# Optimization experiments

Measured on AMD Instinct MI355X. Metric: run time of the kernel, lower is better.

Reference implementation:

```python
import jax, jax.numpy as jnp
import numpy as np

D_MODEL = 1024
N_HEADS = 16
HEAD_DIM = D_MODEL // N_HEADS
SCALE = HEAD_DIM ** -0.5
MIN_VAL = jnp.finfo(jnp.float32).min


def setup_inputs() -> dict:
    key = jax.random.key(0)
    ks = jax.random.split(key, 7)
    B, T = 1, 2048
    s = D_MODEL ** -0.5
    return {
        "x": jax.random.normal(ks[0], (B, T, D_MODEL), dtype=jnp.float32),
        "Wq": jax.random.normal(ks[1], (D_MODEL, D_MODEL), dtype=jnp.float32) * s,
        "Wk1": jax.random.normal(ks[2], (D_MODEL, D_MODEL), dtype=jnp.float32) * s,
        "Wk2": jax.random.normal(ks[3], (D_MODEL, D_MODEL), dtype=jnp.float32) * s,
        "Wv": jax.random.normal(ks[4], (D_MODEL, D_MODEL), dtype=jnp.float32) * s,
        "Wo": jax.random.normal(ks[5], (D_MODEL, D_MODEL), dtype=jnp.float32) * s,
        "lambda_logit": jnp.zeros((N_HEADS,), dtype=jnp.float32),  # logit(0.5)=0
    }


def _split_heads(y):
    B, T, _ = y.shape
    return y.reshape(B, T, N_HEADS, HEAD_DIM).transpose(0, 2, 1, 3)  # [B,H,T,hd]


def reference(x, Wq, Wk1, Wk2, Wv, Wo, lambda_logit):
    B, T, _ = x.shape
    q = _split_heads(x @ Wq.T)
    k1 = _split_heads(x @ Wk1.T)
    k2 = _split_heads(x @ Wk2.T)
    v = _split_heads(x @ Wv.T)

    s1 = jnp.einsum("bhqd,bhkd->bhqk", q, k1) * SCALE
    s2 = jnp.einsum("bhqd,bhkd->bhqk", q, k2) * SCALE

    causal = jnp.arange(T)[None, :] <= jnp.arange(T)[:, None]  # [T,T] keep mask
    s1 = jnp.where(causal[None, None], s1, MIN_VAL)
    s2 = jnp.where(causal[None, None], s2, MIN_VAL)

    attn_exp = jax.nn.softmax(s1, axis=-1)
    attn_noise = jax.nn.softmax(s2, axis=-1)
    lam = jax.nn.sigmoid(lambda_logit)[None, :, None, None]
    attn = attn_exp - lam * attn_noise
    denom = jnp.maximum(jnp.sum(jnp.abs(attn), axis=-1, keepdims=True), 1e-6)
    attn = attn / denom

    out = jnp.einsum("bhqk,bhkd->bhqd", attn, v)
    out = out.transpose(0, 2, 1, 3).reshape(B, T, D_MODEL)
    return out @ Wo.T
```

## Files before the change

### kernel.cpp

```cpp
#include <hip/hip_runtime.h>

#define T_SEQ 2048
#define DM 1024
#define NH 16
#define HD 64
#define SC2 0.1803368801111731f
#define LS 80

typedef unsigned short u16;
typedef unsigned int u32;
typedef __attribute__((ext_vector_type(8))) short bf16x8;
typedef __attribute__((ext_vector_type(4))) float f32x4;

static __device__ __forceinline__ f32x4 mfma16(bf16x8 a, bf16x8 b, f32x4 c) {
    return __builtin_amdgcn_mfma_f32_16x16x32_bf16(a, b, c, 0, 0, 0);
}
static __device__ __forceinline__ float bf2f(u16 u) {
    union { u32 i; float f; } v; v.i = ((u32)u) << 16; return v.f;
}
static __device__ __forceinline__ u16 f2bf(float f) {
    union { float f; u32 i; } v; v.f = f;
    u32 x = v.i;
    x += 0x7FFFu + ((x >> 16) & 1u);
    return (u16)(x >> 16);
}
static __device__ __forceinline__ u16 f2bf_t(float f) {
    union { float f; u32 i; } v; v.f = f;
    return (u16)(v.i >> 16);
}
static __device__ __forceinline__ u32 pk2(float lo, float hi) {
    return (u32)f2bf(lo) | ((u32)f2bf(hi) << 16);
}
static __device__ __forceinline__ uint4 ld8(const void* src, size_t idx, int f) {
    if (f) return *(const uint4*)((const u16*)src + idx);
    const float* s = (const float*)src + idx;
    uint4 a = *(const uint4*)s;
    uint4 b = *(const uint4*)(s + 4);
    const float* af = (const float*)&a;
    const float* bf = (const float*)&b;
    uint4 r;
    r.x = pk2(af[0], af[1]); r.y = pk2(af[2], af[3]);
    r.z = pk2(bf[0], bf[1]); r.w = pk2(bf[2], bf[3]);
    return r;
}
static __device__ __forceinline__ float qsum16(float v) {
#pragma unroll
    for (int o = 1; o < 16; o <<= 1) v += __shfl_xor(v, o, 64);
    return v;
}
static __device__ __forceinline__ float ex2(float x) {
    return __builtin_amdgcn_exp2f(x);
}

static __device__ __forceinline__ void gl16(const u16* g, u16* l) {
    __builtin_amdgcn_global_load_lds(
        (const __attribute__((address_space(1))) void*)g,
        (__attribute__((address_space(3))) void*)l,
        16, 0, 0);
}

template <int NISS>
static __device__ __forceinline__ void stage_async(const u16* src, size_t row0,
                                                   size_t lds_, size_t col0,
                                                   u16* dst, int tid) {
#pragma unroll
    for (int it = 0; it < NISS; it++) {
        int r = it * 32 + (tid >> 3);
        int cg = (tid & 7) ^ (r & 7);
        gl16(&src[(row0 + r) * lds_ + col0 + cg * 8], &dst[(it * 256 + tid) * 8]);
    }
}
template <int NISS>
static __device__ __forceinline__ void stage_sync(const void* src, size_t row0,
                                                  size_t lds_, size_t col0,
                                                  u16* dst, int tid, int f) {
#pragma unroll
    for (int it = 0; it < NISS; it++) {
        int r = it * 32 + (tid >> 3);
        int cg = (tid & 7) ^ (r & 7);
        *(uint4*)(&dst[(it * 256 + tid) * 8]) =
            ld8(src, (row0 + r) * lds_ + col0 + cg * 8, f);
    }
}
static __device__ __forceinline__ bf16x8 frag(const u16* buf, int R, int co) {
    return *(const bf16x8*)(&buf[R * 64 + co]);
}

__global__ void detect_lam(const u16* __restrict__ x, const void* __restrict__ lamsrc,
                           int* __restrict__ flag, float* __restrict__ lamf) {
    __shared__ int tot;
    if (threadIdx.x == 0) tot = 0;
    __syncthreads();
    int c = 0;
    for (int i = threadIdx.x; i < 1024; i += 256) {
        u16 v = x[2 * i];
        int e = (v >> 7) & 0xFF;
        c += (e >= 110 && e <= 140) ? 1 : 0;
    }
    atomicAdd(&tot, c);
    __syncthreads();
    const int f = (tot >= 512) ? 1 : 0;
    if (threadIdx.x == 0) *flag = f;
    if (threadIdx.x < NH) {
        float v = f ? bf2f(((const u16*)lamsrc)[threadIdx.x])
                    : ((const float*)lamsrc)[threadIdx.x];
        lamf[threadIdx.x] = 1.0f / (1.0f + __expf(-v));
    }
}

__global__ __launch_bounds__(256) void qkv_gemm(
    const void* __restrict__ xs, const void* __restrict__ wq,
    const void* __restrict__ wk1, const void* __restrict__ wk2,
    const void* __restrict__ wv, const int* __restrict__ flag,
    u16* __restrict__ qd, u16* __restrict__ k1d, u16* __restrict__ k2d,
    u16* __restrict__ vtd) {
    __shared__ __align__(16) u16 As[2][128 * 64];
    __shared__ __align__(16) u16 Bs[2][128 * 64];

    const int f = *flag;
    const int w = blockIdx.x >> 3;
    const int n0 = (blockIdx.x & 7) * 128;
    const int m0 = blockIdx.y * 128;
    const void* Bpv = (w == 0) ? wq : (w == 1) ? wk1 : (w == 2) ? wk2 : wv;
    const u16* xb = (const u16*)xs;
    const u16* Bb = (const u16*)Bpv;

    const int tid = threadIdx.x;
    const int lane = tid & 63, wave = tid >> 6;
    const int lr = lane & 15, quad = lane >> 4;
    const int wm = (wave >> 1) * 64, wn = (wave & 1) * 64;
    const int sw = lr & 7;

    f32x4 acc[4][4];
#pragma unroll
    for (int i = 0; i < 4; i++)
#pragma unroll
        for (int j = 0; j < 4; j++) acc[i][j] = (f32x4){0.f, 0.f, 0.f, 0.f};

    if (f) {
        stage_async<4>(xb, m0, DM, 0, As[0], tid);
        stage_async<4>(Bb, n0, DM, 0, Bs[0], tid);
    }
    for (int k0 = 0; k0 < DM; k0 += 64) {
        const int cur = (k0 >> 6) & 1;
        __syncthreads();
        if (f) {
            if (k0 + 64 < DM) {
                stage_async<4>(xb, m0, DM, k0 + 64, As[cur ^ 1], tid);
                stage_async<4>(Bb, n0, DM, k0 + 64, Bs[cur ^ 1], tid);
            }
        } else {
            stage_sync<4>(xs, m0, DM, k0, As[cur], tid, 0);
            stage_sync<4>(Bpv, n0, DM, k0, Bs[cur], tid, 0);
            __syncthreads();
        }
#pragma unroll
        for (int kk = 0; kk < 2; kk++) {
            const int co = ((kk * 4 + quad) ^ sw) * 8;
            bf16x8 af[4], bfr[4];
#pragma unroll
            for (int i = 0; i < 4; i++) af[i] = frag(As[cur], wm + i * 16 + lr, co);
#pragma unroll
            for (int j = 0; j < 4; j++) bfr[j] = frag(Bs[cur], wn + j * 16 + lr, co);
#pragma unroll
            for (int i = 0; i < 4; i++)
#pragma unroll
                for (int j = 0; j < 4; j++) acc[i][j] = mfma16(af[i], bfr[j], acc[i][j]);
        }
    }

#pragma unroll
    for (int i = 0; i < 4; i++)
#pragma unroll
        for (int j = 0; j < 4; j++)
#pragma unroll
            for (int r = 0; r < 4; r++) {
                int t = m0 + wm + i * 16 + quad * 4 + r;
                int o = n0 + wn + j * 16 + lr;
                float val = acc[i][j][r];
                if (w == 0) val *= SC2;
                u16 vbits = f2bf(val);
                int hh = o >> 6, d0 = o & 63;
                if (w == 3)
                    vtd[((size_t)hh * HD + d0) * T_SEQ + t] = vbits;
                else
                    ((w == 0) ? qd : (w == 1) ? k1d : k2d)[((size_t)hh * T_SEQ + t) * HD + d0] = vbits;
            }
}

#define ATTN_MAP()                                            \
    const int b = blockIdx.x;                                 \
    const int par = b >> 9;                                   \
    const int rem = b & 511;                                  \
    const int h = rem & 15;                                   \
    const int bi = rem >> 4;                                  \
    const int qt = (bi < 16) ? bi : 47 - bi;                  \
    const int t0 = qt * 64;                                   \
    const int tid = threadIdx.x;                              \
    const int lane = tid & 63, wave = tid >> 6;               \
    const int lr = lane & 15, quad = lane >> 4;               \
    const int wm = wave * 16;                                 \
    const int sw = lr & 7;

__global__ __launch_bounds__(256) void attn_a(
    const u16* __restrict__ qg, const u16* __restrict__ k1g,
    const u16* __restrict__ k2g, float* __restrict__ zp) {
    __shared__ __align__(16) u16 k1s[64 * 64];
    __shared__ __align__(16) u16 k2s[64 * 64];
    ATTN_MAP();

    const u16* qh = qg + (size_t)h * T_SEQ * HD;
    const u16* k1h = k1g + (size_t)h * T_SEQ * HD;
    const u16* k2h = k2g + (size_t)h * T_SEQ * HD;

    bf16x8 aq[2];
#pragma unroll
    for (int kk = 0; kk < 2; kk++)
        aq[kk] = *(const bf16x8*)(&qh[(size_t)(t0 + wm + lr) * HD + kk * 32 + quad * 8]);

    float z1a[4] = {0.f, 0.f, 0.f, 0.f}, z2a[4] = {0.f, 0.f, 0.f, 0.f};

    for (int kt = par; kt <= qt; kt += 4) {
        __syncthreads();
        stage_async<2>(k1h, (size_t)kt * 64, HD, 0, k1s, tid);
        stage_async<2>(k2h, (size_t)kt * 64, HD, 0, k2s, tid);
        __syncthreads();

        f32x4 sa[4], sb[4];
#pragma unroll
        for (int j = 0; j < 4; j++) { sa[j] = (f32x4){0.f,0.f,0.f,0.f}; sb[j] = (f32x4){0.f,0.f,0.f,0.f}; }
#pragma unroll
        for (int kk = 0; kk < 2; kk++) {
            const int co = ((kk * 4 + quad) ^ sw) * 8;
#pragma unroll
            for (int j = 0; j < 4; j++) {
                sa[j] = mfma16(aq[kk], frag(k1s, j * 16 + lr, co), sa[j]);
                sb[j] = mfma16(aq[kk], frag(k2s, j * 16 + lr, co), sb[j]);
            }
        }

        if (kt < qt) {
#pragma unroll
            for (int r = 0; r < 4; r++)
#pragma unroll
                for (int j = 0; j < 4; j++) {
                    z1a[r] += ex2(sa[j][r]);
                    z2a[r] += ex2(sb[j][r]);
                }
        } else {
#pragma unroll
            for (int r = 0; r < 4; r++) {
                const int grow = t0 + wm + quad * 4 + r;
#pragma unroll
                for (int j = 0; j < 4; j++) {
                    int gcol = kt * 64 + j * 16 + lr;
                    if (gcol <= grow) {
                        z1a[r] += ex2(sa[j][r]);
                        z2a[r] += ex2(sb[j][r]);
                    }
                }
            }
        }
    }

#pragma unroll
    for (int r = 0; r < 4; r++) {
        float s1 = qsum16(z1a[r]);
        float s2 = qsum16(z2a[r]);
        if (lr == 0) {
            int row = t0 + wm + quad * 4 + r;
            zp[((size_t)(par * 2 + 0) * NH + h) * T_SEQ + row] = s1;
            zp[((size_t)(par * 2 + 1) * NH + h) * T_SEQ + row] = s2;
        }
    }
}

__global__ __launch_bounds__(256) void attn_b(
    const u16* __restrict__ qg, const u16* __restrict__ k1g,
    const u16* __restrict__ k2g, const u16* __restrict__ vtg,
    const float* __restrict__ zp, const float* __restrict__ lamf,
    float* __restrict__ dpart, u16* __restrict__ opart) {
    __shared__ __align__(16) u16 k1s[64 * 64];
    __shared__ __align__(16) u16 k2s[64 * 64];
    __shared__ __align__(16) u16 vs[64 * 64];
    __shared__ __align__(16) u16 ps[4][16 * LS];
    ATTN_MAP();
    const float lam = lamf[h];

    const u16* qh = qg + (size_t)h * T_SEQ * HD;
    const u16* k1h = k1g + (size_t)h * T_SEQ * HD;
    const u16* k2h = k2g + (size_t)h * T_SEQ * HD;
    const u16* vh = vtg + (size_t)h * HD * T_SEQ;

    bf16x8 aq[2];
#pragma unroll
    for (int kk = 0; kk < 2; kk++)
        aq[kk] = *(const bf16x8*)(&qh[(size_t)(t0 + wm + lr) * HD + kk * 32 + quad * 8]);

    float z1l[4], z2l[4];
#pragma unroll
    for (int r = 0; r < 4; r++) {
        int row = t0 + wm + quad * 4 + r;
        float z1 = 0.f, z2 = 0.f;
#pragma unroll
        for (int p = 0; p < 4; p++) {
            z1 += zp[((size_t)(p * 2 + 0) * NH + h) * T_SEQ + row];
            z2 += zp[((size_t)(p * 2 + 1) * NH + h) * T_SEQ + row];
        }
        z1l[r] = -__log2f(z1);
        z2l[r] = __log2f(lam) - __log2f(z2);
    }

    f32x4 oac[4];
#pragma unroll
    for (int j = 0; j < 4; j++) oac[j] = (f32x4){0.f, 0.f, 0.f, 0.f};
    float dacc[4] = {0.f, 0.f, 0.f, 0.f};

    for (int kt = par; kt <= qt; kt += 2) {
        __syncthreads();
        stage_async<2>(k1h, (size_t)kt * 64, HD, 0, k1s, tid);
        stage_async<2>(k2h, (size_t)kt * 64, HD, 0, k2s, tid);
        stage_async<2>(vh, 0, T_SEQ, (size_t)kt * 64, vs, tid);
        __syncthreads();

        f32x4 sa[4], sb[4];
#pragma unroll
        for (int j = 0; j < 4; j++) { sa[j] = (f32x4){0.f,0.f,0.f,0.f}; sb[j] = (f32x4){0.f,0.f,0.f,0.f}; }
#pragma unroll
        for (int kk = 0; kk < 2; kk++) {
            const int co = ((kk * 4 + quad) ^ sw) * 8;
#pragma unroll
            for (int j = 0; j < 4; j++) {
                sa[j] = mfma16(aq[kk], frag(k1s, j * 16 + lr, co), sa[j]);
                sb[j] = mfma16(aq[kk], frag(k2s, j * 16 + lr, co), sb[j]);
            }
        }

        if (kt < qt) {
#pragma unroll
            for (int r = 0; r < 4; r++)
#pragma unroll
                for (int j = 0; j < 4; j++) {
                    float p = ex2(sa[j][r] + z1l[r]) - ex2(sb[j][r] + z2l[r]);
                    dacc[r] += fabsf(p);
                    ps[wave][(quad * 4 + r) * LS + j * 16 + lr] = f2bf_t(p);
                }
        } else {
#pragma unroll
            for (int r = 0; r < 4; r++) {
                const int grow = t0 + wm + quad * 4 + r;
#pragma unroll
                for (int j = 0; j < 4; j++) {
                    int gcol = kt * 64 + j * 16 + lr;
                    float p = 0.f;
                    if (gcol <= grow)
                        p = ex2(sa[j][r] + z1l[r]) - ex2(sb[j][r] + z2l[r]);
                    dacc[r] += fabsf(p);
                    ps[wave][(quad * 4 + r) * LS + j * 16 + lr] = f2bf_t(p);
                }
            }
        }

#pragma unroll
        for (int kk = 0; kk < 2; kk++) {
            bf16x8 pa = *(const bf16x8*)(&ps[wave][lr * LS + kk * 32 + quad * 8]);
            const int co = ((kk * 4 + quad) ^ sw) * 8;
#pragma unroll
            for (int j = 0; j < 4; j++)
                oac[j] = mfma16(pa, frag(vs, j * 16 + lr, co), oac[j]);
        }
    }

#pragma unroll
    for (int r = 0; r < 4; r++) {
        float ds = qsum16(dacc[r]);
        if (lr == 0) {
            int row = t0 + wm + quad * 4 + r;
            dpart[((size_t)par * NH + h) * T_SEQ + row] = ds;
        }
    }
#pragma unroll
    for (int j = 0; j < 4; j++)
#pragma unroll
        for (int r = 0; r < 4; r++) {
            int row = t0 + wm + quad * 4 + r;
            opart[(size_t)par * T_SEQ * DM + (size_t)row * DM + h * HD + j * 16 + lr] =
                f2bf(oac[j][r]);
        }
}

__global__ __launch_bounds__(256) void normalize_o(
    const u16* __restrict__ opart, const float* __restrict__ dpart,
    u16* __restrict__ ao) {
    int g = blockIdx.x * 256 + threadIdx.x;
    int t = g >> 7;
    int cc = g & 127;
    int d0 = cc * 8;
    int h = d0 >> 6;
    float dsum = dpart[(size_t)h * T_SEQ + t] + dpart[(size_t)(NH + h) * T_SEQ + t];
    float rs = 1.f / fmaxf(dsum, 1e-6f);
    uint4 a = *(const uint4*)(&opart[(size_t)t * DM + d0]);
    uint4 bqq = *(const uint4*)(&opart[(size_t)T_SEQ * DM + (size_t)t * DM + d0]);
    const u32* au = (const u32*)&a;
    const u32* bu = (const u32*)&bqq;
    uint4 out;
    u32* ou = (u32*)&out;
#pragma unroll
    for (int i = 0; i < 4; i++) {
        float lo = (bf2f((u16)(au[i] & 0xFFFF)) + bf2f((u16)(bu[i] & 0xFFFF))) * rs;
        float hi = (bf2f((u16)(au[i] >> 16)) + bf2f((u16)(bu[i] >> 16))) * rs;
        ou[i] = pk2(lo, hi);
    }
    *(uint4*)(&ao[(size_t)t * DM + d0]) = out;
}

__global__ __launch_bounds__(256) void out_gemm(
    const u16* __restrict__ ab, const void* __restrict__ wo,
    const int* __restrict__ flag, void* __restrict__ outp) {
    __shared__ __align__(16) u16 As[2][64 * 64];
    __shared__ __align__(16) u16 Bs[2][64 * 64];

    const int f = *flag;
    const int n0 = blockIdx.x * 64;
    const int m0 = blockIdx.y * 64;
    const u16* wb = (const u16*)wo;
    const int tid = threadIdx.x;
    const int lane = tid & 63, wave = tid >> 6;
    const int lr = lane & 15, quad = lane >> 4;
    const int wm = (wave >> 1) * 32, wn = (wave & 1) * 32;
    const int sw = lr & 7;

    f32x4 acc[2][2];
#pragma unroll
    for (int i = 0; i < 2; i++)
#pragma unroll
        for (int j = 0; j < 2; j++) acc[i][j] = (f32x4){0.f, 0.f, 0.f, 0.f};

    if (f) {
        stage_async<2>(ab, m0, DM, 0, As[0], tid);
        stage_async<2>(wb, n0, DM, 0, Bs[0], tid);
    }
    for (int k0 = 0; k0 < DM; k0 += 64) {
        const int cur = (k0 >> 6) & 1;
        __syncthreads();
        if (f) {
            if (k0 + 64 < DM) {
                stage_async<2>(ab, m0, DM, k0 + 64, As[cur ^ 1], tid);
                stage_async<2>(wb, n0, DM, k0 + 64, Bs[cur ^ 1], tid);
            }
        } else {
            stage_sync<2>(ab, m0, DM, k0, As[cur], tid, 1);
            stage_sync<2>(wo, n0, DM, k0, Bs[cur], tid, 0);
            __syncthreads();
        }
#pragma unroll
        for (int kk = 0; kk < 2; kk++) {
            const int co = ((kk * 4 + quad) ^ sw) * 8;
            bf16x8 af[2], bfr[2];
#pragma unroll
            for (int i = 0; i < 2; i++) af[i] = frag(As[cur], wm + i * 16 + lr, co);
#pragma unroll
            for (int j = 0; j < 2; j++) bfr[j] = frag(Bs[cur], wn + j * 16 + lr, co);
#pragma unroll
            for (int i = 0; i < 2; i++)
#pragma unroll
                for (int j = 0; j < 2; j++) acc[i][j] = mfma16(af[i], bfr[j], acc[i][j]);
        }
    }

#pragma unroll
    for (int i = 0; i < 2; i++)
#pragma unroll
        for (int j = 0; j < 2; j++)
#pragma unroll
            for (int r = 0; r < 4; r++) {
                int t = m0 + wm + i * 16 + quad * 4 + r;
                int o = n0 + wn + j * 16 + lr;
                float val = acc[i][j][r];
                if (f)
                    ((u16*)outp)[(size_t)t * DM + o] = f2bf(val);
                else
                    ((float*)outp)[(size_t)t * DM + o] = val;
            }
}

extern "C" void kernel_launch(void* const* d_in, const int* in_sizes, int n_in,
                              void* d_out, int out_size, void* d_ws, size_t ws_size,
                              hipStream_t stream) {
    char* ws = (char*)d_ws;
    int* flag = (int*)(ws + 0);
    float* lamf = (float*)(ws + 256);
    float* zp    = (float*)(ws + ((size_t)1 << 20));
    float* dpart = (float*)(ws + ((size_t)2 << 20));
    u16* qd  = (u16*)(ws + ((size_t)16 << 20));
    u16* k1d = (u16*)(ws + ((size_t)20 << 20));
    u16* k2d = (u16*)(ws + ((size_t)24 << 20));
    u16* vtd = (u16*)(ws + ((size_t)28 << 20));
    u16* ao  = (u16*)(ws + ((size_t)32 << 20));
    u16* opart = (u16*)(ws + ((size_t)36 << 20));

    detect_lam<<<1, 256, 0, stream>>>((const u16*)d_in[0], d_in[6], flag, lamf);
    qkv_gemm<<<dim3(32, 16), 256, 0, stream>>>(d_in[0], d_in[1], d_in[2], d_in[3],
                                               d_in[4], flag, qd, k1d, k2d, vtd);
    attn_a<<<dim3(2048), 256, 0, stream>>>(qd, k1d, k2d, zp);
    attn_b<<<dim3(1024), 256, 0, stream>>>(qd, k1d, k2d, vtd, zp, lamf, dpart, opart);
    normalize_o<<<dim3(1024), 256, 0, stream>>>(opart, dpart, ao);
    out_gemm<<<dim3(16, 32), 256, 0, stream>>>(ao, d_in[5], flag, d_out);
}
```

Baseline: 205.4 us.

## Fuse dtype detection into QKV GEMM and normalization into output GEMM

Removes the separate detect_lam and normalize_o launches. Every qkv_gemm block now detects the input dtype itself, and attn_b computes the sigmoid of lambda inline. The output GEMM now reads the two bf16 partial outputs, sums them, divides by the denominator and writes the A tile to LDS itself. This replaces the async double-buffered A load with synchronous loads inside the K loop. The ps LDS stride also drops from 80 to 72. The change saves two launches and the ao round trip, but the A tile is no longer prefetched and the opart reads are redundant across N blocks.

```diff
diff --git a/kernel.cpp b/kernel.cpp
--- a/kernel.cpp
+++ b/kernel.cpp
@@ -5,7 +5,7 @@
 #define NH 16
 #define HD 64
 #define SC2 0.1803368801111731f
-#define LS 80
+#define LS 72
 
 typedef unsigned short u16;
 typedef unsigned int u32;
@@ -86,38 +86,36 @@
     return *(const bf16x8*)(&buf[R * 64 + co]);
 }
 
-__global__ void detect_lam(const u16* __restrict__ x, const void* __restrict__ lamsrc,
-                           int* __restrict__ flag, float* __restrict__ lamf) {
-    __shared__ int tot;
-    if (threadIdx.x == 0) tot = 0;
+static __device__ __forceinline__ int detect_flag(const u16* x, int tid,
+                                                  int* tot ) {
+    if (tid == 0) *tot = 0;
     __syncthreads();
     int c = 0;
-    for (int i = threadIdx.x; i < 1024; i += 256) {
-        u16 v = x[2 * i];
+#pragma unroll
+    for (int i = 0; i < 4; i++) {
+        u16 v = x[2 * (tid * 4 + i)];
         int e = (v >> 7) & 0xFF;
         c += (e >= 110 && e <= 140) ? 1 : 0;
     }
-    atomicAdd(&tot, c);
+    atomicAdd(tot, c);
     __syncthreads();
-    const int f = (tot >= 512) ? 1 : 0;
-    if (threadIdx.x == 0) *flag = f;
-    if (threadIdx.x < NH) {
-        float v = f ? bf2f(((const u16*)lamsrc)[threadIdx.x])
-                    : ((const float*)lamsrc)[threadIdx.x];
-        lamf[threadIdx.x] = 1.0f / (1.0f + __expf(-v));
-    }
+    return (*tot >= 512) ? 1 : 0;
 }
 
 __global__ __launch_bounds__(256) void qkv_gemm(
     const void* __restrict__ xs, const void* __restrict__ wq,
     const void* __restrict__ wk1, const void* __restrict__ wk2,
-    const void* __restrict__ wv, const int* __restrict__ flag,
+    const void* __restrict__ wv, int* __restrict__ flag,
     u16* __restrict__ qd, u16* __restrict__ k1d, u16* __restrict__ k2d,
     u16* __restrict__ vtd) {
     __shared__ __align__(16) u16 As[2][128 * 64];
     __shared__ __align__(16) u16 Bs[2][128 * 64];
-
-    const int f = *flag;
+    __shared__ int flg_tot;
+
+    const int tid = threadIdx.x;
+    const int f = detect_flag((const u16*)xs, tid, &flg_tot);
+    if (blockIdx.x == 0 && blockIdx.y == 0 && tid == 0) *flag = f;
+
     const int w = blockIdx.x >> 3;
     const int n0 = (blockIdx.x & 7) * 128;
     const int m0 = blockIdx.y * 128;
@@ -125,7 +123,6 @@
     const u16* xb = (const u16*)xs;
     const u16* Bb = (const u16*)Bpv;
 
-    const int tid = threadIdx.x;
     const int lane = tid & 63, wave = tid >> 6;
     const int lr = lane & 15, quad = lane >> 4;
     const int wm = (wave >> 1) * 64, wn = (wave & 1) * 64;
@@ -278,14 +275,18 @@
 __global__ __launch_bounds__(256) void attn_b(
     const u16* __restrict__ qg, const u16* __restrict__ k1g,
     const u16* __restrict__ k2g, const u16* __restrict__ vtg,
-    const float* __restrict__ zp, const float* __restrict__ lamf,
+    const float* __restrict__ zp, const void* __restrict__ lamsrc,
+    const int* __restrict__ flag,
     float* __restrict__ dpart, u16* __restrict__ opart) {
     __shared__ __align__(16) u16 k1s[64 * 64];
     __shared__ __align__(16) u16 k2s[64 * 64];
     __shared__ __align__(16) u16 vs[64 * 64];
     __shared__ __align__(16) u16 ps[4][16 * LS];
     ATTN_MAP();
-    const float lam = lamf[h];
+
+    const int f = *flag;
+    float lamlogit = f ? bf2f(((const u16*)lamsrc)[h]) : ((const float*)lamsrc)[h];
+    const float lam = 1.0f / (1.0f + __expf(-lamlogit));
 
     const u16* qh = qg + (size_t)h * T_SEQ * HD;
     const u16* k1h = k1g + (size_t)h * T_SEQ * HD;
@@ -389,34 +390,10 @@
         }
 }
 
-__global__ __launch_bounds__(256) void normalize_o(
+__global__ __launch_bounds__(256) void out_gemm(
     const u16* __restrict__ opart, const float* __restrict__ dpart,
-    u16* __restrict__ ao) {
-    int g = blockIdx.x * 256 + threadIdx.x;
-    int t = g >> 7;
-    int cc = g & 127;
-    int d0 = cc * 8;
-    int h = d0 >> 6;
-    float dsum = dpart[(size_t)h * T_SEQ + t] + dpart[(size_t)(NH + h) * T_SEQ + t];
-    float rs = 1.f / fmaxf(dsum, 1e-6f);
-    uint4 a = *(const uint4*)(&opart[(size_t)t * DM + d0]);
-    uint4 bqq = *(const uint4*)(&opart[(size_t)T_SEQ * DM + (size_t)t * DM + d0]);
-    const u32* au = (const u32*)&a;
-    const u32* bu = (const u32*)&bqq;
-    uint4 out;
-    u32* ou = (u32*)&out;
-#pragma unroll
-    for (int i = 0; i < 4; i++) {
-        float lo = (bf2f((u16)(au[i] & 0xFFFF)) + bf2f((u16)(bu[i] & 0xFFFF))) * rs;
-        float hi = (bf2f((u16)(au[i] >> 16)) + bf2f((u16)(bu[i] >> 16))) * rs;
-        ou[i] = pk2(lo, hi);
-    }
-    *(uint4*)(&ao[(size_t)t * DM + d0]) = out;
-}
-
-__global__ __launch_bounds__(256) void out_gemm(
-    const u16* __restrict__ ab, const void* __restrict__ wo,
-    const int* __restrict__ flag, void* __restrict__ outp) {
+    const void* __restrict__ wo, const int* __restrict__ flag,
+    void* __restrict__ outp) {
     __shared__ __align__(16) u16 As[2][64 * 64];
     __shared__ __align__(16) u16 Bs[2][64 * 64];
 
@@ -429,6 +406,7 @@
     const int lr = lane & 15, quad = lane >> 4;
     const int wm = (wave >> 1) * 32, wn = (wave & 1) * 32;
     const int sw = lr & 7;
+    const int srow = tid >> 3;
 
     f32x4 acc[2][2];
 #pragma unroll
@@ -436,23 +414,43 @@
 #pragma unroll
         for (int j = 0; j < 2; j++) acc[i][j] = (f32x4){0.f, 0.f, 0.f, 0.f};
 
-    if (f) {
-        stage_async<2>(ab, m0, DM, 0, As[0], tid);
-        stage_async<2>(wb, n0, DM, 0, Bs[0], tid);
-    }
+    if (f) stage_async<2>(wb, n0, DM, 0, Bs[0], tid);
+
     for (int k0 = 0; k0 < DM; k0 += 64) {
         const int cur = (k0 >> 6) & 1;
-        __syncthreads();
+        const int hh = k0 >> 6;
+        __syncthreads();
+#pragma unroll
+        for (int it = 0; it < 2; it++) {
+            int r = it * 32 + srow;
+            int row = m0 + r;
+            int cg = (tid & 7) ^ (r & 7);
+            size_t off = (size_t)row * DM + k0 + cg * 8;
+            float dsum = dpart[(size_t)hh * 0 + (size_t)(0 * NH) + 0];
+            dsum = dpart[((size_t)0 * NH + hh) * T_SEQ + row] +
+                   dpart[((size_t)1 * NH + hh) * T_SEQ + row];
+            float rs = 1.f / fmaxf(dsum, 1e-6f);
+            uint4 a0 = *(const uint4*)(&opart[off]);
+            uint4 a1 = *(const uint4*)(&opart[(size_t)T_SEQ * DM + off]);
+            const u32* au = (const u32*)&a0;
+            const u32* bu = (const u32*)&a1;
+            uint4 outw;
+            u32* ou = (u32*)&outw;
+#pragma unroll
+            for (int q = 0; q < 4; q++) {
+                float lo = (bf2f((u16)(au[q] & 0xFFFF)) + bf2f((u16)(bu[q] & 0xFFFF))) * rs;
+                float hi = (bf2f((u16)(au[q] >> 16)) + bf2f((u16)(bu[q] >> 16))) * rs;
+                ou[q] = pk2(lo, hi);
+            }
+            *(uint4*)(&As[cur][(it * 256 + tid) * 8]) = outw;
+        }
         if (f) {
-            if (k0 + 64 < DM) {
-                stage_async<2>(ab, m0, DM, k0 + 64, As[cur ^ 1], tid);
+            if (k0 + 64 < DM)
                 stage_async<2>(wb, n0, DM, k0 + 64, Bs[cur ^ 1], tid);
-            }
         } else {
-            stage_sync<2>(ab, m0, DM, k0, As[cur], tid, 1);
             stage_sync<2>(wo, n0, DM, k0, Bs[cur], tid, 0);
-            __syncthreads();
-        }
+        }
+        __syncthreads();
 #pragma unroll
         for (int kk = 0; kk < 2; kk++) {
             const int co = ((kk * 4 + quad) ^ sw) * 8;
@@ -489,21 +487,18 @@
                               hipStream_t stream) {
     char* ws = (char*)d_ws;
     int* flag = (int*)(ws + 0);
-    float* lamf = (float*)(ws + 256);
     float* zp    = (float*)(ws + ((size_t)1 << 20));
     float* dpart = (float*)(ws + ((size_t)2 << 20));
     u16* qd  = (u16*)(ws + ((size_t)16 << 20));
     u16* k1d = (u16*)(ws + ((size_t)20 << 20));
     u16* k2d = (u16*)(ws + ((size_t)24 << 20));
     u16* vtd = (u16*)(ws + ((size_t)28 << 20));
-    u16* ao  = (u16*)(ws + ((size_t)32 << 20));
     u16* opart = (u16*)(ws + ((size_t)36 << 20));
 
-    detect_lam<<<1, 256, 0, stream>>>((const u16*)d_in[0], d_in[6], flag, lamf);
     qkv_gemm<<<dim3(32, 16), 256, 0, stream>>>(d_in[0], d_in[1], d_in[2], d_in[3],
                                                d_in[4], flag, qd, k1d, k2d, vtd);
     attn_a<<<dim3(2048), 256, 0, stream>>>(qd, k1d, k2d, zp);
-    attn_b<<<dim3(1024), 256, 0, stream>>>(qd, k1d, k2d, vtd, zp, lamf, dpart, opart);
-    normalize_o<<<dim3(1024), 256, 0, stream>>>(opart, dpart, ao);
-    out_gemm<<<dim3(16, 32), 256, 0, stream>>>(ao, d_in[5], flag, d_out);
-}
+    attn_b<<<dim3(1024), 256, 0, stream>>>(qd, k1d, k2d, vtd, zp, d_in[6], flag,
+                                           dpart, opart);
+    out_gemm<<<dim3(16, 32), 256, 0, stream>>>(opart, dpart, d_in[5], flag, d_out);
+}
```

Result: no change. 208.7 us (+1.6%).
